# Kernel optimization log

Hardware: AMD Instinct MI355X
Metric: run time of the kernel (lower is better)

## Reference

```python
import jax, jax.numpy as jnp
import numpy as np

T = 100000   # timesteps (hourly)
WIN = 336    # window_size, hardcoded by Tanh(336,336)/Linear(336,out)
OUT = 48     # output_size (2-day horizon)
S = 168      # seasonality_2 (weekly)


def setup_inputs() -> dict:
    key = jax.random.key(0)
    ks = jax.random.split(key, 8)
    # strictly positive series (logs/divisions in forward)
    x = jax.random.uniform(ks[0], (T,), minval=0.5, maxval=1.5, dtype=jnp.float32)
    lvl_coef = jax.random.uniform(ks[1], (), minval=-1.0, maxval=1.0, dtype=jnp.float32)
    seas_coef = jax.random.uniform(ks[2], (), minval=-1.0, maxval=1.0, dtype=jnp.float32)
    # torch init: seasonality param p ~ U(0.65,1.35), used as exp(p); store raw p
    seas_params = jnp.log(jax.random.uniform(ks[3], (S,), minval=0.65, maxval=1.35, dtype=jnp.float32))
    W_tanh = jax.random.normal(ks[4], (WIN, WIN), dtype=jnp.float32) * 0.05
    b_tanh = jnp.zeros((WIN,), dtype=jnp.float32)
    W_out = jax.random.normal(ks[5], (WIN, OUT), dtype=jnp.float32) * 0.05
    b_out = jnp.zeros((OUT,), dtype=jnp.float32)
    return dict(x=x, lvl_coef=lvl_coef, seas_coef=seas_coef, seas_params=seas_params,
                W_tanh=W_tanh, b_tanh=b_tanh, W_out=W_out, b_out=b_out,
                window_size=WIN, output_size=OUT, lvp=50)


def reference(x, lvl_coef, seas_coef, seas_params, W_tanh, b_tanh, W_out, b_out,
              window_size, output_size, lvp):
    std = 0.001
    Tn = x.shape[0]
    a = jax.nn.sigmoid(lvl_coef)       # level smoothing
    g = jax.nn.sigmoid(seas_coef)      # seasonality smoothing
    w0 = jnp.exp(seas_params)          # initial weekly seasonality, [S]
    level0 = x[0] / w0[0]
    # w_seasons[1..S] = [w0[1], ..., w0[S-1], w0[0]] (torch appends w_seasons[0])
    buf0 = jnp.concatenate([w0[1:], w0[:1]])

    def step(carry, xi):
        level, buf = carry
        season = buf[0]                              # w_seasons[i], lag-S recurrence
        new_level = a * xi / season + (1.0 - a) * level
        new_season = g * xi / new_level + (1.0 - g) * season
        buf = jnp.concatenate([buf[1:], new_season[None]])
        return (new_level, buf), (new_level, new_season)

    _, (lvl_seq, new_seasons) = jax.lax.scan(step, (level0, buf0), x[1:])
    levels = jnp.concatenate([level0[None], lvl_seq])          # [T]
    w_all = jnp.concatenate([w0, w0[:1], new_seasons])[:Tn]    # w_seasons[0..T-1]

    # level variation penalty (torch builds it via torch.tensor(list) -> detached)
    lld = jnp.log(levels[1:] / levels[:-1])
    level_var_loss = jax.lax.stop_gradient(jnp.mean((lld[1:] - lld[:-1]) ** 2) * lvp)

    # vectorized sliding windows
    N = Tn - window_size - output_size + 1
    base = jnp.arange(N)
    iw = base[:, None] + jnp.arange(window_size)[None, :]
    il = base[:, None] + window_size + jnp.arange(output_size)[None, :]  # [N, OUT]
    lev = levels[base + window_size][:, None]                            # [N, 1]
    k1, k2 = jax.random.split(jax.random.key(1))
    inputs = jnp.log(x[iw] / (lev * w_all[iw])) + std * jax.random.normal(k1, (N, window_size), dtype=x.dtype)
    labels = jnp.log(x[il] / (lev * w_all[il])) + std * jax.random.normal(k2, (N, output_size), dtype=x.dtype)

    # skip_lstm head: Tanh(336,336) (linear + tanh) -> Linear(336, output_size)
    out = jnp.tanh(inputs @ W_tanh + b_tanh) @ W_out + b_out
    return out, labels, level_var_loss
```

## Files before the change

### kernel.cpp

```cpp
#include <hip/hip_runtime.h>
#include <hip/hip_bf16.h>

#define T_WIN 336
#define T_OUT 48
#define T_S   168
#define BM    128
#define CH    782

typedef __attribute__((ext_vector_type(8))) short short8;
typedef __attribute__((ext_vector_type(4))) float f32x4;

__device__ __forceinline__ short f2bf(float f) {
    union { float f; unsigned u; } v; v.f = f;
    unsigned r = v.u + 0x7FFFu + ((v.u >> 16) & 1u);
    return (short)(r >> 16);
}

template <int CTRL, int RMASK>
__device__ __forceinline__ float dppf(float v) {
    union { float f; int i; } in, out;
    in.f = v;
    out.i = __builtin_amdgcn_update_dpp(0, in.i, CTRL, RMASK, 0xf, true);
    return out.f;
}

__device__ __forceinline__ void st_wt(float* p, float v) {
    __hip_atomic_store(p, v, __ATOMIC_RELAXED, __HIP_MEMORY_SCOPE_AGENT);
}
__device__ __forceinline__ void st_wt_u(unsigned* p, unsigned v) {
    __hip_atomic_store(p, v, __ATOMIC_RELAXED, __HIP_MEMORY_SCOPE_AGENT);
}

__global__ __launch_bounds__(256, 2) void fused_kernel(
    const float* __restrict__ x, const float* __restrict__ lvl_coef,
    const float* __restrict__ seas_coef, const float* __restrict__ seas_params,
    const float* __restrict__ W1, const float* __restrict__ W2,
    const float* __restrict__ b1, const float* __restrict__ b2,
    short* __restrict__ W1F, short* __restrict__ W2F,
    float* __restrict__ w_all, float* __restrict__ levels,
    float* __restrict__ cs, float* __restrict__ outp,
    float* __restrict__ lab, float* __restrict__ lpart,
    int* flags, int T, int N, int NB)
{
    __shared__ float Lsf[512];
    __shared__ __align__(16) short Lbf0[512];
    __shared__ __align__(16) short Lbf1[512];
    __shared__ float llv[BM];
    __shared__ __align__(16) short hs[BM * 72];
    __shared__ __align__(16) short B1s[11 * 4 * 512];
    __shared__ __align__(16) short B2s[6 * 512];
    __shared__ int sh_tk;

    int blk = blockIdx.x;
    int tid = threadIdx.x;
    int* progress  = flags;
    int* prep_done = flags + 32;
    int* ticket    = flags + 64;

    if (blk == 0) {
        if (tid >= 64) return;
        __builtin_amdgcn_s_setprio(3);
        int lane = tid;
        float a = 1.f / (1.f + __expf(-lvl_coef[0]));
        float g = 1.f / (1.f + __expf(-seas_coef[0]));
        float q = 1.f - a, gq = 1.f - g;

        for (int t = lane; t < T_S + 1; t += 64) st_wt(&w_all[t], __expf(seas_params[t % T_S]));
        float lvl = x[0] / __expf(seas_params[0]);
        if (lane == 0) st_wt(&levels[0], lvl);

        float wcur[3];
        #pragma unroll
        for (int i = 0; i < 3; ++i)
            wcur[i] = __expf(seas_params[(1 + 3 * lane + i) % T_S]);

        float f1 = q * q * q;
        float f2 = f1 * f1, f4 = f2 * f2, f8 = f4 * f4;
        float lnq = __logf(q);
        float P15 = __expf(3.f * (float)((lane & 15) + 1) * lnq);
        float P31 = __expf(3.f * (float)((lane & 31) + 1) * lnq);
        float pw3l = __expf(3.f * (float)lane * lnq);

        int j0 = 3 * lane;

        auto do_chunk = [&](const float* xvv, float* lev) {
            float rr[3];
            #pragma unroll
            for (int i = 0; i < 3; ++i) rr[i] = a * xvv[i] * __builtin_amdgcn_rcpf(wcur[i]);
            float S = fmaf(q, fmaf(q, rr[0], rr[1]), rr[2]);
            S = fmaf(f1, dppf<0x111, 0xf>(S), S);
            S = fmaf(f2, dppf<0x112, 0xf>(S), S);
            S = fmaf(f4, dppf<0x114, 0xf>(S), S);
            S = fmaf(f8, dppf<0x118, 0xf>(S), S);
            S = fmaf(P15, dppf<0x142, 0xa>(S), S);
            S = fmaf(P31, dppf<0x143, 0xc>(S), S);
            float E = dppf<0x138, 0xf>(S);
            float lv = fmaf(pw3l, lvl, E);
            #pragma unroll
            for (int i = 0; i < 3; ++i) { lv = fmaf(q, lv, rr[i]); lev[i] = lv; }
            { union { float f; int i; } uu; uu.i = __builtin_amdgcn_readlane(__builtin_bit_cast(int, lev[2]), 55); lvl = uu.f; }
            #pragma unroll
            for (int i = 0; i < 3; ++i)
                wcur[i] = fmaf(gq, wcur[i], g * xvv[i] * __builtin_amdgcn_rcpf(lev[i]));
        };

        float xg[4][3], xh[4][3], x2[4][3];
        #pragma unroll
        for (int u = 0; u < 4; ++u)
            #pragma unroll
            for (int i = 0; i < 3; ++i) {
                xg[u][i] = x[1 + T_S * u + j0 + i];
                xh[u][i] = x[1 + T_S * (4 + u) + j0 + i];
            }

        const float* px = x + 1 + 8 * T_S + j0;
        float* pl = levels + 1 + j0;
        float* pw = w_all + 1 + T_S + j0;

        for (int grp = 0; grp < 148; ++grp) {
            if (grp && (grp & 7) == 0 && lane == 0) {
                asm volatile("s_waitcnt vmcnt(0)" ::: "memory");
                __hip_atomic_store(progress, grp, __ATOMIC_RELAXED, __HIP_MEMORY_SCOPE_AGENT);
            }

            if (grp < 146) {
                #pragma unroll
                for (int u = 0; u < 4; ++u)
                    #pragma unroll
                    for (int i = 0; i < 3; ++i)
                        x2[u][i] = px[u * T_S + i];
            } else {
                #pragma unroll
                for (int u = 0; u < 4; ++u)
                    #pragma unroll
                    for (int i = 0; i < 3; ++i) {
                        int t = 1 + T_S * (4 * (grp + 2) + u) + j0 + i;
                        x2[u][i] = x[min(t, T - 1)];
                    }
            }
            px += 4 * T_S;

            #pragma unroll
            for (int u = 0; u < 4; ++u) {
                float lev[3];
                do_chunk(xg[u], lev);
                #pragma unroll
                for (int i = 0; i < 3; ++i) {
                    st_wt(&pl[u * T_S + i], lev[i]);
                    st_wt(&pw[u * T_S + i], wcur[i]);
                }
            }
            pl += 4 * T_S; pw += 4 * T_S;
            #pragma unroll
            for (int u = 0; u < 4; ++u)
                #pragma unroll
                for (int i = 0; i < 3; ++i) { xg[u][i] = xh[u][i]; xh[u][i] = x2[u][i]; }
        }

        #pragma unroll
        for (int u = 0; u < 4; ++u) {
            int c = 592 + u;
            if (c * T_S >= T - 1) break;
            int len = (T - 1) - T_S * c; if (len > T_S) len = T_S;
            float lev[3];
            do_chunk(xg[u], lev);
            #pragma unroll
            for (int i = 0; i < 3; ++i) {
                if (j0 + i < len) {
                    st_wt(&pl[u * T_S + i], lev[i]);
                    st_wt(&pw[u * T_S + i], wcur[i]);
                }
            }
        }
        asm volatile("s_waitcnt vmcnt(0)" ::: "memory");
        if (lane == 0)
            __hip_atomic_store(progress, 1000, __ATOMIC_RELAXED, __HIP_MEMORY_SCOPE_AGENT);
        return;
    }

    if (blk <= 302) {
        if (blk >= 301) {
            int k = (blk - 301) * 256 + tid;
            if (k < T_WIN) {
                float s = 0.f;
                for (int j = 0; j < T_WIN; ++j) s += W1[j * T_WIN + k];
                st_wt(&cs[k], s);
            }
        } else if (blk >= 265) {
            int d = (blk - 265) * 256 + tid;
            int j2 = d & 3, lane = (d >> 2) & 63, f = d >> 8;
            int ct2 = f % 3, rest = f / 3;
            int kt2 = rest & 1, c = rest >> 1;
            int k = c * 64 + kt2 * 32 + (lane >> 4) * 8 + 2 * j2;
            int o = ct2 * 16 + (lane & 15);
            unsigned short lo = 0, hi = 0;
            if (k     < T_WIN) lo = (unsigned short)f2bf(W2[k * T_OUT + o]);
            if (k + 1 < T_WIN) hi = (unsigned short)f2bf(W2[(k + 1) * T_OUT + o]);
            st_wt_u(&((unsigned*)W2F)[d], ((unsigned)hi << 16) | (unsigned)lo);
        } else {
            int d = (blk - 1) * 256 + tid;
            int j2 = d & 3, lane = (d >> 2) & 63, f = d >> 8;
            int ct = f & 3, rest = f >> 2;
            int kt = rest % 11, c = rest / 11;
            int k = kt * 32 + (lane >> 4) * 8 + 2 * j2;
            int col = c * 64 + ct * 16 + (lane & 15);
            unsigned short lo = 0, hi = 0;
            if (col < T_WIN) {
                if (k     < T_WIN) lo = (unsigned short)f2bf(W1[k * T_WIN + col]);
                if (k + 1 < T_WIN) hi = (unsigned short)f2bf(W1[(k + 1) * T_WIN + col]);
            }
            st_wt_u(&((unsigned*)W1F)[d], ((unsigned)hi << 16) | (unsigned)lo);
        }
        __syncthreads();
        if (tid == 0)
            __hip_atomic_fetch_add(prep_done, 1, __ATOMIC_RELAXED, __HIP_MEMORY_SCOPE_AGENT);
    }

    if (tid < 64) {
        while (__hip_atomic_load(prep_done, __ATOMIC_RELAXED, __HIP_MEMORY_SCOPE_AGENT) < 302)
            __builtin_amdgcn_s_sleep(16);
    }
    __syncthreads();

    int lane = tid & 63, wv = tid >> 6;
    int lr = lane & 15, lq = lane >> 4;
    int rw = wv * 32;
    int last_seen = 0;
    int NT = NB + 128;

    for (;;) {
        __syncthreads();
        if (tid == 0) sh_tk = atomicAdd(ticket, 1);
        __syncthreads();
        int tk = sh_tk;
        if (tk >= NT) return;

        int need_t = (tk < NB) ? (tk * BM + 512 + 128) : ((tk - NB) * CH + CH + 2 + 128);
        if (need_t > T) need_t = T;
        int req = (need_t + 670) / 672;
        if (last_seen < req) {
            if (tid < 64) {
                while (__hip_atomic_load(progress, __ATOMIC_RELAXED, __HIP_MEMORY_SCOPE_AGENT) < req)
                    __builtin_amdgcn_s_sleep(32);
            }
            __syncthreads();
            last_seen = req;
        }

        if (tk >= NB) {
            float* ls  = (float*)hs;
            float* red = (float*)(hs + 4096);
            int lb = tk - NB;
            int lo = lb * CH;
            int n = T - lo; if (n > CH + 2) n = CH + 2;
            for (int i = tid; i < n; i += 256) ls[i] = __logf(levels[lo + i]);
            __syncthreads();
            float s = 0.f;
            int dmax = (T - 2) - lo; if (dmax > CH) dmax = CH;
            for (int i = tid; i < dmax; i += 256) {
                float d = ls[i + 2] - 2.f * ls[i + 1] + ls[i];
                s = fmaf(d, d, s);
            }
            red[tid] = s;
            __syncthreads();
            for (int w = 128; w > 0; w >>= 1) {
                if (tid < w) red[tid] += red[tid + w];
                __syncthreads();
            }
            if (tid == 0) lpart[lb] = red[0];
            continue;
        }

        int n0 = tk * BM;
        float C = __logf(levels[min(n0 + T_WIN, T - 1)]);

        for (int i = tid; i < 512; i += 256) {
            int t = n0 + i;
            float v = (t < T) ? (__logf(x[t]) - __logf(w_all[t]) - C) : 0.f;
            Lsf[i] = v;
            Lbf0[i] = f2bf(v);
        }
        for (int i = tid; i < BM; i += 256) {
            int t = n0 + i + T_WIN;
            llv[i] = (t < T) ? (__logf(levels[t]) - C) : 0.f;
        }
        __syncthreads();
        for (int i = tid; i < 512; i += 256) Lbf1[i] = (i < 511) ? Lbf0[i + 1] : (short)0;
        __syncthreads();

        for (int u2 = tid; u2 < BM * T_OUT; u2 += 256) {
            int row = u2 / T_OUT, j = u2 - row * T_OUT;
            int nn = n0 + row;
            if (nn < N) lab[(size_t)nn * T_OUT + j] = Lsf[row + T_WIN + j] - llv[row];
        }

        const short* abase = ((lr & 1) ? Lbf1 : Lbf0) + rw + (lr & ~1);
        short8 af[11][2];
        #pragma unroll
        for (int kt = 0; kt < 11; ++kt) {
            #pragma unroll
            for (int mt = 0; mt < 2; ++mt) {
                const int* ip = (const int*)(abase + mt * 16 + kt * 32 + lq * 8);
                union { short8 s; int i[4]; } u;
                u.i[0] = ip[0]; u.i[1] = ip[1]; u.i[2] = ip[2]; u.i[3] = ip[3];
                af[kt][mt] = u.s;
            }
        }

        f32x4 zero4 = {0.f, 0.f, 0.f, 0.f};
        f32x4 acc2[2][3];
        #pragma unroll
        for (int mt = 0; mt < 2; ++mt)
            #pragma unroll
            for (int ct = 0; ct < 3; ++ct) acc2[mt][ct] = zero4;

        #pragma unroll 1
        for (int c = 0; c < 6; ++c) {
            __syncthreads();

            const char* g1 = (const char*)(W1F + (size_t)c * 11 * 4 * 512);
            for (int seg = wv; seg < 44; seg += 4) {
                __builtin_amdgcn_global_load_lds(
                    (const __attribute__((address_space(1))) unsigned int*)(g1 + seg * 1024 + lane * 16),
                    (__attribute__((address_space(3))) unsigned int*)((char*)B1s + seg * 1024),
                    16, 0, 0);
            }
            const char* g2 = (const char*)(W2F + (size_t)c * 6 * 512);
            for (int seg = wv; seg < 6; seg += 4) {
                __builtin_amdgcn_global_load_lds(
                    (const __attribute__((address_space(1))) unsigned int*)(g2 + seg * 1024 + lane * 16),
                    (__attribute__((address_space(3))) unsigned int*)((char*)B2s + seg * 1024),
                    16, 0, 0);
            }
            float b1v[4], csv[4];
            #pragma unroll
            for (int ct = 0; ct < 4; ++ct) {
                int col = c * 64 + ct * 16 + lr;
                b1v[ct] = (col < T_WIN) ? b1[col] : 0.f;
                csv[ct] = (col < T_WIN) ? cs[col] : 0.f;
            }
            __syncthreads();

            f32x4 acc1[2][4];
            #pragma unroll
            for (int mt = 0; mt < 2; ++mt)
                #pragma unroll
                for (int ct = 0; ct < 4; ++ct) acc1[mt][ct] = zero4;

            #pragma unroll
            for (int kt = 0; kt < 11; ++kt) {
                #pragma unroll
                for (int ct = 0; ct < 4; ++ct) {
                    short8 bf = *(const short8*)&B1s[((kt * 4 + ct) * 64 + lane) * 8];
                    acc1[0][ct] = __builtin_amdgcn_mfma_f32_16x16x32_bf16(af[kt][0], bf, acc1[0][ct], 0, 0, 0);
                    acc1[1][ct] = __builtin_amdgcn_mfma_f32_16x16x32_bf16(af[kt][1], bf, acc1[1][ct], 0, 0, 0);
                }
            }

            #pragma unroll
            for (int mt = 0; mt < 2; ++mt)
                #pragma unroll
                for (int ct = 0; ct < 4; ++ct)
                    #pragma unroll
                    for (int r = 0; r < 4; ++r) {
                        int row = rw + mt * 16 + lq * 4 + r;
                        float pre = acc1[mt][ct][r] + b1v[ct] - llv[row] * csv[ct];
                        float e = __expf(2.f * pre);
                        float h = 1.f - 2.f * __builtin_amdgcn_rcpf(e + 1.f);
                        hs[row * 72 + ct * 16 + lr] = f2bf(h);
                    }

            #pragma unroll
            for (int kt2 = 0; kt2 < 2; ++kt2) {
                short8 a2[2];
                #pragma unroll
                for (int mt = 0; mt < 2; ++mt)
                    a2[mt] = *(const short8*)&hs[(rw + mt * 16 + lr) * 72 + kt2 * 32 + lq * 8];
                #pragma unroll
                for (int ct2 = 0; ct2 < 3; ++ct2) {
                    short8 bf2 = *(const short8*)&B2s[((kt2 * 3 + ct2) * 64 + lane) * 8];
                    acc2[0][ct2] = __builtin_amdgcn_mfma_f32_16x16x32_bf16(a2[0], bf2, acc2[0][ct2], 0, 0, 0);
                    acc2[1][ct2] = __builtin_amdgcn_mfma_f32_16x16x32_bf16(a2[1], bf2, acc2[1][ct2], 0, 0, 0);
                }
            }
        }

        float b2v[3];
        #pragma unroll
        for (int ct2 = 0; ct2 < 3; ++ct2) b2v[ct2] = b2[ct2 * 16 + lr];
        #pragma unroll
        for (int mt = 0; mt < 2; ++mt)
            #pragma unroll
            for (int ct2 = 0; ct2 < 3; ++ct2)
                #pragma unroll
                for (int r = 0; r < 4; ++r) {
                    int row = n0 + rw + mt * 16 + lq * 4 + r;
                    if (row < N)
                        outp[(size_t)row * T_OUT + ct2 * 16 + lr] = acc2[mt][ct2][r] + b2v[ct2];
                }
    }
}

__global__ __launch_bounds__(128) void loss2_kernel(
    const float* __restrict__ part, const int* __restrict__ lvp,
    float* __restrict__ out_loss, int T)
{
    __shared__ float red[128];
    red[threadIdx.x] = part[threadIdx.x];
    __syncthreads();
    for (int w = 64; w > 0; w >>= 1) {
        if (threadIdx.x < (unsigned)w) red[threadIdx.x] += red[threadIdx.x + w];
        __syncthreads();
    }
    if (threadIdx.x == 0) out_loss[0] = red[0] * (float)lvp[0] / (float)(T - 2);
}

extern "C" void kernel_launch(void* const* d_in, const int* in_sizes, int n_in,
                              void* d_out, int out_size, void* d_ws, size_t ws_size,
                              hipStream_t stream) {
    const float* x    = (const float*)d_in[0];
    const float* lvlc = (const float*)d_in[1];
    const float* seac = (const float*)d_in[2];
    const float* sp   = (const float*)d_in[3];
    const float* W1   = (const float*)d_in[4];
    const float* b1   = (const float*)d_in[5];
    const float* W2   = (const float*)d_in[6];
    const float* b2   = (const float*)d_in[7];
    const int*   lvp  = (const int*)d_in[10];

    int T = in_sizes[0];
    int N = T - T_WIN - T_OUT + 1;
    int NB = (N + BM - 1) / BM;

    short* W1F    = (short*)d_ws;
    short* W2F    = W1F + 264 * 512;
    float* w_all  = (float*)(W2F + 36 * 512);
    float* levels = w_all + T + 192;
    float* cs     = levels + T;
    float* lpart  = cs + 352;
    int*   flagsp = (int*)(lpart + 128);

    float* outp  = (float*)d_out;
    float* lab   = outp + (size_t)N * T_OUT;
    float* lossp = lab + (size_t)N * T_OUT;

    hipMemsetAsync((void*)flagsp, 0, 384, stream);

    fused_kernel<<<512, 256, 0, stream>>>(x, lvlc, seac, sp, W1, W2, b1, b2,
                                          W1F, W2F, w_all, levels, cs,
                                          outp, lab, lpart, flagsp, T, N, NB);
    loss2_kernel<<<1, 128, 0, stream>>>(lpart, lvp, lossp, T);
}
```

Before: 229.5 us.

## Interleave loss tiles with GEMM tiles, use release stores, replace memset with kernel

Result: no change. 230.3 us (+0.4%).

```diff
diff --git a/kernel.cpp b/kernel.cpp
--- a/kernel.cpp
+++ b/kernel.cpp
@@ -29,6 +29,10 @@
 }
 __device__ __forceinline__ void st_wt_u(unsigned* p, unsigned v) {
     __hip_atomic_store(p, v, __ATOMIC_RELAXED, __HIP_MEMORY_SCOPE_AGENT);
+}
+
+__global__ void init_flags(int* flags) {
+    if (threadIdx.x < 3) flags[threadIdx.x * 32] = 0;
 }
 
 __global__ __launch_bounds__(256, 2) void fused_kernel(
@@ -65,9 +69,9 @@
         float g = 1.f / (1.f + __expf(-seas_coef[0]));
         float q = 1.f - a, gq = 1.f - g;
 
-        for (int t = lane; t < T_S + 1; t += 64) st_wt(&w_all[t], __expf(seas_params[t % T_S]));
+        for (int t = lane; t < T_S + 1; t += 64) w_all[t] = __expf(seas_params[t % T_S]);
         float lvl = x[0] / __expf(seas_params[0]);
-        if (lane == 0) st_wt(&levels[0], lvl);
+        if (lane == 0) levels[0] = lvl;
 
         float wcur[3];
         #pragma unroll
@@ -118,10 +122,8 @@
         float* pw = w_all + 1 + T_S + j0;
 
         for (int grp = 0; grp < 148; ++grp) {
-            if (grp && (grp & 7) == 0 && lane == 0) {
-                asm volatile("s_waitcnt vmcnt(0)" ::: "memory");
-                __hip_atomic_store(progress, grp, __ATOMIC_RELAXED, __HIP_MEMORY_SCOPE_AGENT);
-            }
+            if (grp && (grp & 7) == 0 && lane == 0)
+                __hip_atomic_store(progress, grp, __ATOMIC_RELEASE, __HIP_MEMORY_SCOPE_AGENT);
 
             if (grp < 146) {
                 #pragma unroll
@@ -146,8 +148,8 @@
                 do_chunk(xg[u], lev);
                 #pragma unroll
                 for (int i = 0; i < 3; ++i) {
-                    st_wt(&pl[u * T_S + i], lev[i]);
-                    st_wt(&pw[u * T_S + i], wcur[i]);
+                    pl[u * T_S + i] = lev[i];
+                    pw[u * T_S + i] = wcur[i];
                 }
             }
             pl += 4 * T_S; pw += 4 * T_S;
@@ -167,14 +169,13 @@
             #pragma unroll
             for (int i = 0; i < 3; ++i) {
                 if (j0 + i < len) {
-                    st_wt(&pl[u * T_S + i], lev[i]);
-                    st_wt(&pw[u * T_S + i], wcur[i]);
+                    pl[u * T_S + i] = lev[i];
+                    pw[u * T_S + i] = wcur[i];
                 }
             }
         }
-        asm volatile("s_waitcnt vmcnt(0)" ::: "memory");
         if (lane == 0)
-            __hip_atomic_store(progress, 1000, __ATOMIC_RELAXED, __HIP_MEMORY_SCOPE_AGENT);
+            __hip_atomic_store(progress, 1000, __ATOMIC_RELEASE, __HIP_MEMORY_SCOPE_AGENT);
         return;
     }
 
@@ -235,7 +236,12 @@
         int tk = sh_tk;
         if (tk >= NT) return;
 
-        int need_t = (tk < NB) ? (tk * BM + 512 + 128) : ((tk - NB) * CH + CH + 2 + 128);
+        int sev = tk / 7;
+        bool isl = (tk % 7 == 6) && (sev < 128);
+        int tile = isl ? (NB + sev) : (tk - min(sev, 128));
+
+        int need_t = (tile < NB) ? (tile * BM + 512 + 128)
+                                 : ((tile - NB) * CH + CH + 2 + 128);
         if (need_t > T) need_t = T;
         int req = (need_t + 670) / 672;
         if (last_seen < req) {
@@ -247,10 +253,10 @@
             last_seen = req;
         }
 
-        if (tk >= NB) {
+        if (tile >= NB) {
             float* ls  = (float*)hs;
             float* red = (float*)(hs + 4096);
-            int lb = tk - NB;
+            int lb = tile - NB;
             int lo = lb * CH;
             int n = T - lo; if (n > CH + 2) n = CH + 2;
             for (int i = tid; i < n; i += 256) ls[i] = __logf(levels[lo + i]);
@@ -271,7 +277,7 @@
             continue;
         }
 
-        int n0 = tk * BM;
+        int n0 = tile * BM;
         float C = __logf(levels[min(n0 + T_WIN, T - 1)]);
 
         for (int i = tid; i < 512; i += 256) {
@@ -444,8 +450,7 @@
     float* lab   = outp + (size_t)N * T_OUT;
     float* lossp = lab + (size_t)N * T_OUT;
 
-    hipMemsetAsync((void*)flagsp, 0, 384, stream);
-
+    init_flags<<<1, 64, 0, stream>>>(flagsp);
     fused_kernel<<<512, 256, 0, stream>>>(x, lvlc, seac, sp, W1, W2, b1, b2,
                                           W1F, W2F, w_all, levels, cs,
                                           outp, lab, lpart, flagsp, T, N, NB);
```
